# Kernel optimization log

Hardware: AMD Instinct MI355X
Metric: run time of the kernel (lower is better)

## Reference

```python
import jax, jax.numpy as jnp
import numpy as np

EPS = 1e-12  # matches torch F.normalize eps and utils.get_diagonal threshold


def _geteig(feats, K):
    # feats: [B, C, H, W]
    B, C, H, W = feats.shape
    nH, nW = H // 4, W // 4
    # bilinear, align_corners=False (half-pixel centers) == jax.image.resize 'bilinear'
    f = jax.image.resize(feats, (B, C, nH, nW), method='bilinear')
    f = f.reshape(B, C, nH * nW).transpose(0, 2, 1)  # [B, N, C]
    norm = jnp.linalg.norm(f, axis=-1, keepdims=True)
    f = f / jnp.maximum(norm, EPS)  # L2-normalize per pixel

    def per_sample(x):  # x: [N, C]
        Wm = x @ x.T                       # cosine similarity [N, N]
        Wm = Wm * (Wm > 0)                 # keep positive affinities
        Wm = Wm / Wm.max()
        Wm = jax.lax.stop_gradient(Wm)     # original detaches before eigsh
        d = Wm.sum(axis=1)                 # degree (row sums), as in utils.get_diagonal
        d = jnp.where(d < EPS, 1.0, d)
        inv_sqrt = 1.0 / jnp.sqrt(d)
        L = jnp.diag(d) - Wm               # unnormalized Laplacian
        # generalized problem L v = lam D v  <=>  eigh of D^-1/2 L D^-1/2
        Ln = inv_sqrt[:, None] * L * inv_sqrt[None, :]
        Ln = 0.5 * (Ln + Ln.T)             # enforce symmetry for stability
        evals = jnp.linalg.eigh(Ln)[0]     # ascending
        return evals[:K]                   # K smallest (eigsh sigma=0, which='LM')

    return jax.vmap(per_sample)(f)  # [B, K]


def setup_inputs() -> dict:
    key = jax.random.key(0)
    feats = jax.random.normal(key, (8, 3, 160, 160), dtype=jnp.float32)
    return {"feats": feats, "K": 10}


def reference(feats, K):
    lan1 = _geteig(feats[:, :1], K)    # channel 0 -> [B, K]
    lan2 = _geteig(feats[:, 1:2], K)   # channel 1 -> [B, K]
    # NOTE: faithful to original bug: feats[:2:3] slices the BATCH dim -> [1, C, H, W]
    lan3 = _geteig(feats[:2:3], K)     # [1, K], broadcasts in the MSE below
    loss = jnp.mean((lan1 - lan2) ** 2)
    loss = loss + jnp.mean((lan1 - lan3) ** 2)
    loss = loss + jnp.mean((lan2 - lan3) ** 2)
    return loss * 5
```

## Files before the change

kernel.cpp:

```cpp
#include <hip/hip_runtime.h>
#include <math.h>

#define N16 1600
#define M 32
#define XSZ 51200
#define BIS_IT 28
#define EPSF 1e-12f


__device__ void taps1d(int o, int* lo, int* hi, float* wsum, float w[8]) {
  int l = 4 * o - 2, h = 4 * o + 5;
  if (l < 0) l = 0;
  if (h > 159) h = 159;
  float c = 4.f * o + 1.5f, s = 0.f;
  for (int x = l; x <= h; ++x) {
    float ww = 1.f - fabsf((float)x - c) * 0.25f;
    w[x - l] = ww;
    s += ww;
  }
  *lo = l; *hi = h; *wsum = s;
}

__global__ void __launch_bounds__(256)
k_resize(const float* __restrict__ in, float* __restrict__ rz) {
  const int bx = blockIdx.x, t = threadIdx.x;
  int map = bx / 7;
  int o = (bx % 7) * 256 + t;
  if (o >= N16) return;
  int oy = o / 40, ox = o % 40;
  int ly, hy, lx, hx; float sy, sx; float wy[8], wx[8];
  taps1d(oy, &ly, &hy, &sy, wy);
  taps1d(ox, &lx, &hx, &sx, wx);
  const float* src = in + (size_t)map * 160 * 160;
  float acc = 0.f;
  for (int y = ly; y <= hy; ++y) {
    float a = 0.f;
    const float* row = src + y * 160;
    for (int x = lx; x <= hx; ++x) a += wx[x - lx] * row[x];
    acc += wy[y - ly] * a;
  }
  rz[map * N16 + o] = acc / (sy * sx);
}

__global__ void __launch_bounds__(256)
k_prep(const float* __restrict__ rz, float* __restrict__ F,
       int* __restrict__ flags) {
  __shared__ int sp[256];
  __shared__ int sn[256];
  const int bx = blockIdx.x, t = threadIdx.x;
  if (bx < 16) {
    int b = bx >> 1, c = bx & 1;
    const float* m = rz + (b * 3 + c) * N16;
    int cp = 0, cn = 0;
    for (int o = t; o < N16; o += 256) {
      float v = m[o];
      cp += (v > 0.f);
      cn += (v < 0.f);
    }
    sp[t] = cp; sn[t] = cn;
    __syncthreads();
    for (int s = 128; s > 0; s >>= 1) {
      if (t < s) { sp[t] += sp[t + s]; sn[t] += sn[t + s]; }
      __syncthreads();
    }
    if (t == 0) flags[bx] = (sp[0] == 0 || sn[0] == 0) ? 1 : 0;
  } else {
    int n = (bx - 16) * 256 + t;
    if (n < N16) {
      float x = rz[n], y = rz[N16 + n], z = rz[2 * N16 + n];
      float nrm = sqrtf(x * x + y * y + z * z);
      float s = 1.f / fmaxf(nrm, EPSF);
      F[n * 3 + 0] = x * s;
      F[n * 3 + 1] = y * s;
      F[n * 3 + 2] = z * s;
    }
  }
}

__global__ void __launch_bounds__(256)
k_degree(const float* __restrict__ F, float* __restrict__ R,
         float* __restrict__ G4f, float* __restrict__ X0) {
  __shared__ float Fl[4800];
  __shared__ float red[256];
  const int bx = blockIdx.x, t = threadIdx.x;
  for (int s = t; s < 4800; s += 256) Fl[s] = F[s];
  __syncthreads();
  int rl = t >> 4, jt = t & 15;
  int i = bx * 16 + rl;
  float fx = Fl[i * 3], fy = Fl[i * 3 + 1], fz = Fl[i * 3 + 2];
  float s = 0.f;
#pragma unroll 8
  for (int j = jt; j < N16; j += 16) {
    float w = fx * Fl[j * 3] + fy * Fl[j * 3 + 1] + fz * Fl[j * 3 + 2];
    if (w > 0.f) s += w;
  }
  red[t] = s;
  __syncthreads();
  for (int st = 8; st > 0; st >>= 1) {
    if (jt < st) red[t] += red[t + st];
    __syncthreads();
  }
  if (jt == 0) {
    float d = red[t];
    if (d < EPSF) d = 1.f;
    float r = rsqrtf(d);
    R[i] = r;
    G4f[i * 4 + 0] = r * fx;
    G4f[i * 4 + 1] = r * fy;
    G4f[i * 4 + 2] = r * fz;
    G4f[i * 4 + 3] = 0.f;
  }
  for (int e = t; e < 512; e += 256) {
    int n = bx * 16 + (e >> 5);
    int k = e & 31;
    unsigned u = ((unsigned)n * 2654435761u) ^ ((unsigned)k * 0x9E3779B9u);
    u = u * 1664525u + 1013904223u;
    u ^= u >> 16; u *= 2246822519u; u ^= u >> 13;
    X0[n * M + k] = ((float)(u >> 8) * (1.f / 8388608.f)) - 1.f;
  }
}

__global__ void __launch_bounds__(256)
k_mv(const float* __restrict__ F, const float4* __restrict__ G4,
     const float* __restrict__ R, const float* __restrict__ Xin,
     float* __restrict__ Xout) {
  __shared__ float Ws[2][1088];
  __shared__ float XsT[2][1088];
  __shared__ float Red[16 * 264];
  const int bx = blockIdx.x, t = threadIdx.x;
  const int ig = bx >> 1, kh = bx & 1;
  const int i0 = ig * 16, kbase = kh * 16;
  const int rg = t & 3, kg = (t >> 2) & 3, jg = t >> 4;
  const int sj = t >> 2, sq = t & 3;
  const int wil = t & 15, wjg = t >> 4;
  const float fx = F[(i0 + wil) * 3 + 0];
  const float fy = F[(i0 + wil) * 3 + 1];
  const float fz = F[(i0 + wil) * 3 + 2];

  float acc[4][4];
#pragma unroll
  for (int r = 0; r < 4; ++r)
#pragma unroll
    for (int kk = 0; kk < 4; ++kk) acc[r][kk] = 0.f;

  {
    float4 xs = ((const float4*)Xin)[(size_t)sj * 8 + kh * 4 + sq];
    XsT[0][(sq * 4 + 0) * 68 + sj] = xs.x;
    XsT[0][(sq * 4 + 1) * 68 + sj] = xs.y;
    XsT[0][(sq * 4 + 2) * 68 + sj] = xs.z;
    XsT[0][(sq * 4 + 3) * 68 + sj] = xs.w;
#pragma unroll
    for (int q = 0; q < 4; ++q) {
      float4 g = G4[wjg + 16 * q];
      Ws[0][wil * 68 + wjg + 16 * q] =
          fmaxf(fx * g.x + fy * g.y + fz * g.z, 0.f);
    }
  }
  __syncthreads();

  for (int c = 0; c < 25; ++c) {
    const int cur = c & 1, nxt = cur ^ 1;
    float4 xs = {0.f, 0.f, 0.f, 0.f};
    float4 ga[4];
    if (c < 24) {
      const int jb = (c + 1) * 64;
      xs = ((const float4*)Xin)[(size_t)(jb + sj) * 8 + kh * 4 + sq];
#pragma unroll
      for (int q = 0; q < 4; ++q) ga[q] = G4[jb + wjg + 16 * q];
    }
    {
      const int jq = jg * 4;
      float4 wv[4], xv[4];
#pragma unroll
      for (int r = 0; r < 4; ++r)
        wv[r] = *(const float4*)&Ws[cur][(rg * 4 + r) * 68 + jq];
#pragma unroll
      for (int kk = 0; kk < 4; ++kk)
        xv[kk] = *(const float4*)&XsT[cur][(kg * 4 + kk) * 68 + jq];
#pragma unroll
      for (int r = 0; r < 4; ++r)
#pragma unroll
        for (int kk = 0; kk < 4; ++kk)
          acc[r][kk] += wv[r].x * xv[kk].x + wv[r].y * xv[kk].y +
                        wv[r].z * xv[kk].z + wv[r].w * xv[kk].w;
    }
    if (c < 24) {
      XsT[nxt][(sq * 4 + 0) * 68 + sj] = xs.x;
      XsT[nxt][(sq * 4 + 1) * 68 + sj] = xs.y;
      XsT[nxt][(sq * 4 + 2) * 68 + sj] = xs.z;
      XsT[nxt][(sq * 4 + 3) * 68 + sj] = xs.w;
#pragma unroll
      for (int q = 0; q < 4; ++q)
        Ws[nxt][wil * 68 + wjg + 16 * q] =
            fmaxf(fx * ga[q].x + fy * ga[q].y + fz * ga[q].z, 0.f);
    }
    __syncthreads();
  }

#pragma unroll
  for (int r = 0; r < 4; ++r)
#pragma unroll
    for (int kk = 0; kk < 4; ++kk)
      Red[jg * 264 + (rg * 4 + r) * 16 + (kg * 4 + kk)] = acc[r][kk];
  __syncthreads();
  {
    const int il = t >> 4, kl = t & 15;
    float sv = 0.f;
#pragma unroll
    for (int g = 0; g < 16; ++g) sv += Red[g * 264 + il * 16 + kl];
    const int gi = i0 + il, gk = kbase + kl;
    Xout[(size_t)gi * 32 + gk] =
        0.5f * Xin[(size_t)gi * 32 + gk] + 0.5f * R[gi] * sv;
  }
}

__global__ void __launch_bounds__(256)
k_gram(const float* __restrict__ Xa, const float* __restrict__ Xb,
       float* __restrict__ GPp) {
  __shared__ float sA[2048];
  __shared__ float sB[2048];
  const int bx = blockIdx.x, t = threadIdx.x;
  float acc[4] = {0.f, 0.f, 0.f, 0.f};
  for (int c = 0; c < 5; ++c) {
    const int j0 = bx * 320 + c * 64;
    __syncthreads();
    for (int s = t; s < 2048; s += 256) {
      sA[s] = Xa[(size_t)j0 * 32 + s];
      sB[s] = Xb[(size_t)j0 * 32 + s];
    }
    __syncthreads();
#pragma unroll
    for (int s = 0; s < 4; ++s) {
      int e = s * 256 + t;
      int a = e >> 5, b = e & 31;
      float sum = 0.f;
#pragma unroll 8
      for (int jl = 0; jl < 64; ++jl) sum += sA[jl * 32 + a] * sB[jl * 32 + b];
      acc[s] += sum;
    }
  }
#pragma unroll
  for (int s = 0; s < 4; ++s) GPp[(size_t)bx * 1024 + s * 256 + t] = acc[s];
}

__global__ void __launch_bounds__(256)
k_apply(const float* __restrict__ GPp, const float* __restrict__ Xin,
        float* __restrict__ Xout) {
  __shared__ float Gm[32 * 33];
  const int bx = blockIdx.x, t = threadIdx.x;
#pragma unroll
  for (int u = 0; u < 4; ++u) {
    int e = t + u * 256;
    float g = 0.f;
#pragma unroll
    for (int p = 0; p < 5; ++p) g += GPp[p * 1024 + e];
    Gm[(e >> 5) * 33 + (e & 31)] = g;
  }
  const int r = t >> 5, l = t & 31;
  const int row = bx * 8 + r;
  float x = Xin[(size_t)row * M + l];
  __syncthreads();
  if (t < 64) {
    for (int k = 0; k < 32; ++k) {
      if (t == k) Gm[k * 33 + k] = sqrtf(fmaxf(Gm[k * 33 + k], 1e-30f));
      float piv = Gm[k * 33 + k];
      if (t > k && t < 32) Gm[t * 33 + k] /= piv;
#pragma unroll
      for (int u = 0; u < 16; ++u) {
        int e = t + u * 64;
        int i = e >> 5, j = e & 31;
        if (i > k && j > k && j <= i)
          Gm[i * 33 + j] -= Gm[i * 33 + k] * Gm[j * 33 + k];
      }
    }
  }
  __syncthreads();
  const int half = t & 32;
  float y = 0.f;
  for (int k = 0; k < 32; ++k) {
    float gkl = Gm[k * 33 + l];
    float contrib = (l < k) ? y * gkl : 0.f;
#pragma unroll
    for (int o = 16; o; o >>= 1) contrib += __shfl_xor(contrib, o, 64);
    float xk = __shfl(x, half + k, 64);
    float yk = (xk - contrib) / Gm[k * 33 + k];
    if (l == k) y = yk;
  }
  Xout[(size_t)row * M + l] = y;
}

__device__ __forceinline__ float wred(float v) {
#pragma unroll
  for (int o = 32; o; o >>= 1) v += __shfl_xor(v, o, 64);
  return v;
}
__device__ __forceinline__ float wredmin(float v) {
#pragma unroll
  for (int o = 32; o; o >>= 1) v = fminf(v, __shfl_xor(v, o, 64));
  return v;
}
__device__ __forceinline__ float wredmax(float v) {
#pragma unroll
  for (int o = 32; o; o >>= 1) v = fmaxf(v, __shfl_xor(v, o, 64));
  return v;
}

__global__ void __launch_bounds__(64)
k_rr(const float* __restrict__ GPp, const int* __restrict__ flags,
     const int* __restrict__ Kptr, float* __restrict__ out) {
  __shared__ float Bs[1088];
  __shared__ float part[1024];
  __shared__ float vvs[32];
  __shared__ float uus[32];
  __shared__ float dd[32];
  __shared__ float ee[32];
  __shared__ float ee2[32];
  __shared__ float evs[32];
  const int t = threadIdx.x;
#pragma unroll
  for (int u = 0; u < 16; ++u) {
    int e = t + u * 64;
    float g = 0.f;
#pragma unroll
    for (int p = 0; p < 5; ++p) g += GPp[p * 1024 + e];
    part[e] = g;
  }
  if (t < 32) Bs[1056 + t] = 0.f;
  __syncthreads();
#pragma unroll
  for (int u = 0; u < 16; ++u) {
    int e = t + u * 64;
    int i = e >> 5, j = e & 31;
    Bs[i * 33 + j] = 0.5f * (part[e] + part[j * 32 + i]);
  }
  __syncthreads();
  for (int k = 0; k <= 29; ++k) {
    const int m = 31 - k;
    float xi = (t < m) ? Bs[(k + 1 + t) * 33 + k] : 0.f;
    float nx2 = wred(xi * xi);
    float x0 = __shfl(xi, 0, 64);
    if (nx2 < 1e-28f) {
      if (t == 0) ee[k] = x0;
      __syncthreads();
      continue;
    }
    float alpha = (x0 >= 0.f) ? -sqrtf(nx2) : sqrtf(nx2);
    float h = nx2 - alpha * x0;
    float vi = (t < m) ? ((t == 0) ? (xi - alpha) : xi) : 0.f;
    if (t < 32) vvs[t] = vi;
    if (t == 0) ee[k] = alpha;
    __syncthreads();
    float pi = 0.f;
    if (t < m) {
      const float* rowp = &Bs[(k + 1 + t) * 33 + (k + 1)];
#pragma unroll
      for (int j = 0; j < 31; ++j) pi += rowp[j] * vvs[j];
      pi /= h;
    }
    float vp = wred((t < 32) ? vi * pi : 0.f);
    float Kc = vp / (2.f * h);
    if (t < 32) uus[t] = (t < m) ? (pi - Kc * vi) : 0.f;
    __syncthreads();
#pragma unroll
    for (int u = 0; u < 16; ++u) {
      int e = t + u * 64;
      int i = e >> 5, j = e & 31;
      if (i < m && j < m)
        Bs[(k + 1 + i) * 33 + (k + 1 + j)] -= vvs[i] * uus[j] + uus[i] * vvs[j];
    }
    __syncthreads();
  }
  if (t < 32) dd[t] = Bs[t * 33 + t];
  if (t == 0) { ee[30] = Bs[31 * 33 + 30]; ee[31] = 0.f; }
  __syncthreads();
  if (t < 32) ee2[t] = (t < 31) ? ee[t] * ee[t] : 0.f;
  __syncthreads();
  float lo, hi;
  {
    int tt = t & 31;
    float di = dd[tt];
    float r = 0.f;
    if (tt > 0) r += fabsf(ee[tt - 1]);
    if (tt < 31) r += fabsf(ee[tt]);
    lo = wredmin(di - r) - 1e-6f;
    hi = wredmax(di + r) + 1e-6f;
  }
  if (t < 32) {
    float ddr[32], ee2r[31];
#pragma unroll
    for (int i2 = 0; i2 < 32; ++i2) ddr[i2] = dd[i2];
#pragma unroll
    for (int i2 = 0; i2 < 31; ++i2) ee2r[i2] = ee2[i2];
    float a = lo, b = hi;
    for (int it = 0; it < BIS_IT; ++it) {
      float mid = 0.5f * (a + b);
      float q = ddr[0] - mid;
      int cnt = (q < 0.f) ? 1 : 0;
#pragma unroll
      for (int i = 1; i < 32; ++i) {
        float den = q;
        float ad = fabsf(den);
        den = (ad < 1e-30f) ? ((den < 0.f) ? -1e-30f : 1e-30f) : den;
        q = ddr[i] - mid - ee2r[i - 1] * __builtin_amdgcn_rcpf(den);
        cnt += (q < 0.f) ? 1 : 0;
      }
      if (cnt <= t) a = mid; else b = mid;
    }
    evs[t] = 0.5f * (a + b);
  }
  __syncthreads();
  if (t == 0) {
    int K = Kptr ? *Kptr : 10;
    if (K < 1) K = 10;
    if (K > 32) K = 32;
    float t12 = 0.f, t13 = 0.f, t23 = 0.f;
    for (int b = 0; b < 8; ++b) {
      float f1 = flags[b * 2 + 0] ? 1.f : 0.f;
      float f2 = flags[b * 2 + 1] ? 1.f : 0.f;
      for (int k = 0; k < K; ++k) {
        float v1 = (k == 0) ? 0.f : (k == 1 ? f1 : 1.f);
        float v2 = (k == 0) ? 0.f : (k == 1 ? f2 : 1.f);
        float m3 = 2.f - 2.f * evs[31 - k];
        t12 += (v1 - v2) * (v1 - v2);
        t13 += (v1 - m3) * (v1 - m3);
        t23 += (v2 - m3) * (v2 - m3);
      }
    }
    out[0] = 5.f * (t12 + t13 + t23) / (8.f * (float)K);
  }
}

extern "C" void kernel_launch(void* const* d_in, const int* in_sizes, int n_in,
                              void* d_out, int out_size, void* d_ws, size_t ws_size,
                              hipStream_t stream) {
  const float* feats = (const float*)d_in[0];
  const int* Kptr = (n_in > 1) ? (const int*)d_in[1] : nullptr;
  float* ws = (float*)d_ws;
  float* RZ = ws;
  float* F  = ws + 38400;
  float* G4f = ws + 43200;
  float* R  = ws + 49600;
  int* FLAGS = (int*)(ws + 51200);
  float* GP = ws + 51264;
  float* XB = ws + 51264 + 15360;
  float* bufs[4] = {XB, XB + XSZ, XB + 2 * XSZ, XB + 3 * XSZ};
  const float4* G4 = (const float4*)G4f;
  float* outp = (float*)d_out;

  k_resize<<<dim3(168), dim3(256), 0, stream>>>(feats, RZ);
  k_prep<<<dim3(23), dim3(256), 0, stream>>>(RZ, F, FLAGS);
  k_degree<<<dim3(100), dim3(256), 0, stream>>>(F, R, G4f, bufs[0]);

  const float* cur = bufs[0];
  for (int m = 1; m <= 10; ++m) {
    float* o = bufs[1 + m % 3];
    k_mv<<<dim3(200), dim3(256), 0, stream>>>(F, G4, R, cur, o);
    cur = o;
  }
  k_gram<<<dim3(5), dim3(256), 0, stream>>>(cur, cur, GP);
  k_apply<<<dim3(200), dim3(256), 0, stream>>>(GP, cur, bufs[0]);
  cur = bufs[0];
  for (int m = 11; m <= 20; ++m) {
    float* o = bufs[1 + m % 3];
    k_mv<<<dim3(200), dim3(256), 0, stream>>>(F, G4, R, cur, o);
    cur = o;
  }
  k_gram<<<dim3(5), dim3(256), 0, stream>>>(cur, cur, GP + 5120);
  k_apply<<<dim3(200), dim3(256), 0, stream>>>(GP + 5120, cur, bufs[0]);
  k_mv<<<dim3(200), dim3(256), 0, stream>>>(F, G4, R, bufs[0], bufs[1]);
  k_gram<<<dim3(5), dim3(256), 0, stream>>>(bufs[0], bufs[1], GP + 10240);
  k_rr<<<dim3(1), dim3(64), 0, stream>>>(GP + 10240, FLAGS, Kptr, outp);
}
```

Baseline: 589.9 us.

## Halve k_mv row tile to double grid; register-resident Householder tridiagonalization in k_rr

The k_mv matvec kernel now processes 8 rows per block instead of 16, doubling the grid from 200 to 400 blocks so more CUs are busy on the 1600-row problem. The cost is that each block re-streams the full X panel for half the rows, doubling total X and G loads. Separately, the single-wave k_rr tridiagonalization keeps each row in registers. It computes full 32-wide dot products and rank-2 updates with one row per thread instead of strided shared-memory loops with bounds checks. This trades extra register pressure and redundant arithmetic on already-reduced rows for fewer index calculations.

```diff
diff --git a/kernel.cpp b/kernel.cpp
--- a/kernel.cpp
+++ b/kernel.cpp
@@ -124,22 +124,22 @@
 k_mv(const float* __restrict__ F, const float4* __restrict__ G4,
      const float* __restrict__ R, const float* __restrict__ Xin,
      float* __restrict__ Xout) {
-  __shared__ float Ws[2][1088];
+  __shared__ float Ws[2][544];
   __shared__ float XsT[2][1088];
-  __shared__ float Red[16 * 264];
+  __shared__ float Red[16 * 136];
   const int bx = blockIdx.x, t = threadIdx.x;
   const int ig = bx >> 1, kh = bx & 1;
-  const int i0 = ig * 16, kbase = kh * 16;
+  const int i0 = ig * 8, kbase = kh * 16;
   const int rg = t & 3, kg = (t >> 2) & 3, jg = t >> 4;
   const int sj = t >> 2, sq = t & 3;
-  const int wil = t & 15, wjg = t >> 4;
+  const int wil = t & 7, wjg = t >> 3;
   const float fx = F[(i0 + wil) * 3 + 0];
   const float fy = F[(i0 + wil) * 3 + 1];
   const float fz = F[(i0 + wil) * 3 + 2];
 
-  float acc[4][4];
-#pragma unroll
-  for (int r = 0; r < 4; ++r)
+  float acc[2][4];
+#pragma unroll
+  for (int r = 0; r < 2; ++r)
 #pragma unroll
     for (int kk = 0; kk < 4; ++kk) acc[r][kk] = 0.f;
 
@@ -150,9 +150,9 @@
     XsT[0][(sq * 4 + 2) * 68 + sj] = xs.z;
     XsT[0][(sq * 4 + 3) * 68 + sj] = xs.w;
 #pragma unroll
-    for (int q = 0; q < 4; ++q) {
-      float4 g = G4[wjg + 16 * q];
-      Ws[0][wil * 68 + wjg + 16 * q] =
+    for (int q = 0; q < 2; ++q) {
+      float4 g = G4[wjg + 32 * q];
+      Ws[0][wil * 68 + wjg + 32 * q] =
           fmaxf(fx * g.x + fy * g.y + fz * g.z, 0.f);
     }
   }
@@ -161,24 +161,24 @@
   for (int c = 0; c < 25; ++c) {
     const int cur = c & 1, nxt = cur ^ 1;
     float4 xs = {0.f, 0.f, 0.f, 0.f};
-    float4 ga[4];
+    float4 ga[2];
     if (c < 24) {
       const int jb = (c + 1) * 64;
       xs = ((const float4*)Xin)[(size_t)(jb + sj) * 8 + kh * 4 + sq];
 #pragma unroll
-      for (int q = 0; q < 4; ++q) ga[q] = G4[jb + wjg + 16 * q];
+      for (int q = 0; q < 2; ++q) ga[q] = G4[jb + wjg + 32 * q];
     }
     {
       const int jq = jg * 4;
-      float4 wv[4], xv[4];
-#pragma unroll
-      for (int r = 0; r < 4; ++r)
-        wv[r] = *(const float4*)&Ws[cur][(rg * 4 + r) * 68 + jq];
+      float4 wv[2], xv[4];
+#pragma unroll
+      for (int r = 0; r < 2; ++r)
+        wv[r] = *(const float4*)&Ws[cur][(rg * 2 + r) * 68 + jq];
 #pragma unroll
       for (int kk = 0; kk < 4; ++kk)
         xv[kk] = *(const float4*)&XsT[cur][(kg * 4 + kk) * 68 + jq];
 #pragma unroll
-      for (int r = 0; r < 4; ++r)
+      for (int r = 0; r < 2; ++r)
 #pragma unroll
         for (int kk = 0; kk < 4; ++kk)
           acc[r][kk] += wv[r].x * xv[kk].x + wv[r].y * xv[kk].y +
@@ -190,24 +190,24 @@
       XsT[nxt][(sq * 4 + 2) * 68 + sj] = xs.z;
       XsT[nxt][(sq * 4 + 3) * 68 + sj] = xs.w;
 #pragma unroll
-      for (int q = 0; q < 4; ++q)
-        Ws[nxt][wil * 68 + wjg + 16 * q] =
+      for (int q = 0; q < 2; ++q)
+        Ws[nxt][wil * 68 + wjg + 32 * q] =
             fmaxf(fx * ga[q].x + fy * ga[q].y + fz * ga[q].z, 0.f);
     }
     __syncthreads();
   }
 
 #pragma unroll
-  for (int r = 0; r < 4; ++r)
+  for (int r = 0; r < 2; ++r)
 #pragma unroll
     for (int kk = 0; kk < 4; ++kk)
-      Red[jg * 264 + (rg * 4 + r) * 16 + (kg * 4 + kk)] = acc[r][kk];
-  __syncthreads();
-  {
+      Red[jg * 136 + (rg * 2 + r) * 16 + (kg * 4 + kk)] = acc[r][kk];
+  __syncthreads();
+  if (t < 128) {
     const int il = t >> 4, kl = t & 15;
     float sv = 0.f;
 #pragma unroll
-    for (int g = 0; g < 16; ++g) sv += Red[g * 264 + il * 16 + kl];
+    for (int g = 0; g < 16; ++g) sv += Red[g * 136 + il * 16 + kl];
     const int gi = i0 + il, gk = kbase + kl;
     Xout[(size_t)gi * 32 + gk] =
         0.5f * Xin[(size_t)gi * 32 + gk] + 0.5f * R[gi] * sv;
@@ -308,9 +308,9 @@
 __global__ void __launch_bounds__(64)
 k_rr(const float* __restrict__ GPp, const int* __restrict__ flags,
      const int* __restrict__ Kptr, float* __restrict__ out) {
-  __shared__ float Bs[1088];
+  __shared__ float Bs[1056];
   __shared__ float part[1024];
-  __shared__ float vvs[32];
+  __shared__ float vgs[32];
   __shared__ float uus[32];
   __shared__ float dd[32];
   __shared__ float ee[32];
@@ -325,7 +325,6 @@
     for (int p = 0; p < 5; ++p) g += GPp[p * 1024 + e];
     part[e] = g;
   }
-  if (t < 32) Bs[1056 + t] = 0.f;
   __syncthreads();
 #pragma unroll
   for (int u = 0; u < 16; ++u) {
@@ -335,10 +334,9 @@
   }
   __syncthreads();
   for (int k = 0; k <= 29; ++k) {
-    const int m = 31 - k;
-    float xi = (t < m) ? Bs[(k + 1 + t) * 33 + k] : 0.f;
+    float xi = (t > k && t < 32) ? Bs[t * 33 + k] : 0.f;
     float nx2 = wred(xi * xi);
-    float x0 = __shfl(xi, 0, 64);
+    float x0 = __shfl(xi, k + 1, 64);
     if (nx2 < 1e-28f) {
       if (t == 0) ee[k] = x0;
       __syncthreads();
@@ -346,27 +344,33 @@
     }
     float alpha = (x0 >= 0.f) ? -sqrtf(nx2) : sqrtf(nx2);
     float h = nx2 - alpha * x0;
-    float vi = (t < m) ? ((t == 0) ? (xi - alpha) : xi) : 0.f;
-    if (t < 32) vvs[t] = vi;
+    float vg = (t == k + 1) ? (xi - alpha) : xi;
+    if (t < 32) vgs[t] = vg;
     if (t == 0) ee[k] = alpha;
     __syncthreads();
+    float rv[32], vgr[32];
     float pi = 0.f;
-    if (t < m) {
-      const float* rowp = &Bs[(k + 1 + t) * 33 + (k + 1)];
-#pragma unroll
-      for (int j = 0; j < 31; ++j) pi += rowp[j] * vvs[j];
+    if (t < 32) {
+#pragma unroll
+      for (int c = 0; c < 32; ++c) rv[c] = Bs[t * 33 + c];
+#pragma unroll
+      for (int c = 0; c < 32; ++c) vgr[c] = vgs[c];
+#pragma unroll
+      for (int c = 0; c < 32; ++c) pi += rv[c] * vgr[c];
       pi /= h;
     }
-    float vp = wred((t < 32) ? vi * pi : 0.f);
+    float vp = wred((t < 32) ? vg * pi : 0.f);
     float Kc = vp / (2.f * h);
-    if (t < 32) uus[t] = (t < m) ? (pi - Kc * vi) : 0.f;
-    __syncthreads();
-#pragma unroll
-    for (int u = 0; u < 16; ++u) {
-      int e = t + u * 64;
-      int i = e >> 5, j = e & 31;
-      if (i < m && j < m)
-        Bs[(k + 1 + i) * 33 + (k + 1 + j)] -= vvs[i] * uus[j] + uus[i] * vvs[j];
+    float ug = (t > k && t < 32) ? (pi - Kc * vg) : 0.f;
+    if (t < 32) uus[t] = ug;
+    __syncthreads();
+    if (t < 32) {
+      float ugr[32];
+#pragma unroll
+      for (int c = 0; c < 32; ++c) ugr[c] = uus[c];
+#pragma unroll
+      for (int c = 0; c < 32; ++c)
+        Bs[t * 33 + c] = rv[c] - (vg * ugr[c] + ug * vgr[c]);
     }
     __syncthreads();
   }
@@ -454,7 +458,7 @@
   const float* cur = bufs[0];
   for (int m = 1; m <= 10; ++m) {
     float* o = bufs[1 + m % 3];
-    k_mv<<<dim3(200), dim3(256), 0, stream>>>(F, G4, R, cur, o);
+    k_mv<<<dim3(400), dim3(256), 0, stream>>>(F, G4, R, cur, o);
     cur = o;
   }
   k_gram<<<dim3(5), dim3(256), 0, stream>>>(cur, cur, GP);
@@ -462,12 +466,12 @@
   cur = bufs[0];
   for (int m = 11; m <= 20; ++m) {
     float* o = bufs[1 + m % 3];
-    k_mv<<<dim3(200), dim3(256), 0, stream>>>(F, G4, R, cur, o);
+    k_mv<<<dim3(400), dim3(256), 0, stream>>>(F, G4, R, cur, o);
     cur = o;
   }
   k_gram<<<dim3(5), dim3(256), 0, stream>>>(cur, cur, GP + 5120);
   k_apply<<<dim3(200), dim3(256), 0, stream>>>(GP + 5120, cur, bufs[0]);
-  k_mv<<<dim3(200), dim3(256), 0, stream>>>(F, G4, R, bufs[0], bufs[1]);
+  k_mv<<<dim3(400), dim3(256), 0, stream>>>(F, G4, R, bufs[0], bufs[1]);
   k_gram<<<dim3(5), dim3(256), 0, stream>>>(bufs[0], bufs[1], GP + 10240);
   k_rr<<<dim3(1), dim3(64), 0, stream>>>(GP + 10240, FLAGS, Kptr, outp);
 }
```

After: 542.6 us. 1.09x faster.
